# Kernel optimization log

Hardware: AMD Instinct MI355X
Metric: run time of the kernel (lower is better)

The kernel has to match this reference:

```python
import jax, jax.numpy as jnp
import numpy as np

N = 100000        # nodes
E = 1600000       # edges (before self-loops)
IN_CH = 256       # input features
HEADS = 8         # conv1 heads; per-head dim also 8 (GATConv(in, heads, heads=heads))
HID = 8
NCLASS = 64
SLOPE = 0.2       # PyG leaky_relu negative slope


def _gat_conv(x, edge_index, W, att_src, att_dst, bias, heads, ch, concat):
    """PyG GATConv (eval mode): gather -> leaky_relu score -> segment softmax -> scatter."""
    n = x.shape[0]
    src, dst = edge_index[0], edge_index[1]
    h = (x @ W).reshape(n, heads, ch)                      # [N, H, C]
    a_src = jnp.einsum('nhc,hc->nh', h, att_src)           # [N, H]
    a_dst = jnp.einsum('nhc,hc->nh', h, att_dst)
    alpha = jax.nn.leaky_relu(a_src[src] + a_dst[dst], SLOPE)  # [E, H]
    # segment softmax over destination node
    amax = jax.ops.segment_max(alpha, dst, num_segments=n)     # [N, H]
    ex = jnp.exp(alpha - amax[dst])
    denom = jax.ops.segment_sum(ex, dst, num_segments=n)
    coef = ex / (denom[dst] + 1e-16)                           # [E, H]
    out = jax.ops.segment_sum(coef[:, :, None] * h[src], dst, num_segments=n)  # [N, H, C]
    if concat:
        out = out.reshape(n, heads * ch)
    else:
        out = out.mean(axis=1)
    return out + bias


def _add_self_loops(edge_index, n):
    loop = jnp.arange(n, dtype=edge_index.dtype)
    return jnp.concatenate([edge_index, jnp.stack([loop, loop])], axis=1)


def setup_inputs() -> dict:
    key = jax.random.key(0)
    ks = jax.random.split(key, 10)
    g = lambda k, shp, s: (jax.random.normal(k, shp, jnp.float32) * s)
    return {
        'x': jax.random.normal(ks[0], (N, IN_CH), jnp.float32),
        'edge_index': jax.random.randint(ks[1], (2, E), 0, N, dtype=jnp.int64),
        'W1': g(ks[2], (IN_CH, HEADS * HID), 1.0 / np.sqrt(IN_CH)),
        'att_src1': g(ks[3], (HEADS, HID), 0.3),
        'att_dst1': g(ks[4], (HEADS, HID), 0.3),
        'b1': jnp.zeros((HEADS * HID,), jnp.float32),
        'W2': g(ks[5], (HEADS * HID, NCLASS), 1.0 / np.sqrt(HEADS * HID)),
        'att_src2': g(ks[6], (1, NCLASS), 0.3),
        'att_dst2': g(ks[7], (1, NCLASS), 0.3),
        'b2': jnp.zeros((NCLASS,), jnp.float32),
    }


def reference(x, edge_index, W1, att_src1, att_dst1, b1, W2, att_src2, att_dst2, b2):
    ei = _add_self_loops(edge_index, x.shape[0])
    h = jax.nn.elu(_gat_conv(x, ei, W1, att_src1, att_dst1, b1, HEADS, HID, True))
    # dropout is a no-op in eval mode
    h = _gat_conv(h, ei, W2, att_src2, att_dst2, b2, 1, NCLASS, False)
    return jax.nn.log_softmax(h, axis=-1)
```

## Files before the change

kernel.cpp:

```cpp
#include <hip/hip_runtime.h>
#include <hip/hip_bf16.h>

#define LRELU_SLOPE 0.2f
#define NBUK 256
#define BCAP 9728
#define CH2 6144

typedef unsigned int uint;
typedef unsigned short ushort;
typedef short bt8 __attribute__((ext_vector_type(8)));
typedef float fx4 __attribute__((ext_vector_type(4)));

__device__ __forceinline__ ushort f2bf(float f) {
    uint u = __float_as_uint(f);
    return (ushort)((u + 0x7FFF + ((u >> 16) & 1)) >> 16);
}
__device__ __forceinline__ float bf2f(ushort h) {
    return __uint_as_float(((uint)h) << 16);
}

#define ACC8(e, hv) \
    acc[0] += (e) * bf2f((ushort)((hv).x & 0xffff)); \
    acc[1] += (e) * bf2f((ushort)((hv).x >> 16));    \
    acc[2] += (e) * bf2f((ushort)((hv).y & 0xffff)); \
    acc[3] += (e) * bf2f((ushort)((hv).y >> 16));    \
    acc[4] += (e) * bf2f((ushort)((hv).z & 0xffff)); \
    acc[5] += (e) * bf2f((ushort)((hv).z >> 16));    \
    acc[6] += (e) * bf2f((ushort)((hv).w & 0xffff)); \
    acc[7] += (e) * bf2f((ushort)((hv).w >> 16));

#define EDGE_H8(sjv, LIVE) { \
    uint4 hv = *(const uint4*)(HB + (size_t)(sjv) * 64 + ol * 8); \
    float h0 = bf2f((ushort)(hv.x & 0xffff)), h1 = bf2f((ushort)(hv.x >> 16)); \
    float h2 = bf2f((ushort)(hv.y & 0xffff)), h3 = bf2f((ushort)(hv.y >> 16)); \
    float h4 = bf2f((ushort)(hv.z & 0xffff)), h5 = bf2f((ushort)(hv.z >> 16)); \
    float h6 = bf2f((ushort)(hv.w & 0xffff)), h7 = bf2f((ushort)(hv.w >> 16)); \
    float dt = h0*w0.x + h1*w0.y + h2*w0.z + h3*w0.w \
             + h4*w1.x + h5*w1.y + h6*w1.z + h7*w1.w; \
    float a_ = dt + adh; a_ = a_ > 0.f ? a_ : LRELU_SLOPE * a_; \
    float e = __expf(a_); \
    if (!(LIVE)) e = 0.f; \
    dsum += e; \
    acc[0] += e*h0; acc[1] += e*h1; acc[2] += e*h2; acc[3] += e*h3; \
    acc[4] += e*h4; acc[5] += e*h5; acc[6] += e*h6; acc[7] += e*h7; }

__global__ __launch_bounds__(256) void prep_init(
    const float* __restrict__ W1, const float* __restrict__ W2,
    ushort* __restrict__ WT1, ushort* __restrict__ WT2, int* __restrict__ pcur)
{
    int t = threadIdx.x;
    int idx = blockIdx.x * 256 + t;
    if (blockIdx.x == 0) pcur[t] = t * BCAP;
    if (idx < 64 * 256) {
        int c = idx >> 8, k = idx & 255;
        WT1[idx] = f2bf(W1[k * 64 + c]);
    }
    int i2 = idx - 64 * 256;
    if (i2 >= 0 && i2 < 64 * 64) {
        int c = i2 >> 6, k = i2 & 63;
        WT2[i2] = f2bf(W2[k * 64 + c]);
    }
}

__device__ __forceinline__ void partition_body(
    int bid, const int* __restrict__ ei, int E_, int ET,
    int* __restrict__ pcur, uint* __restrict__ pairs,
    int* lcnt, int* lsc, int* lplace, int* gpos)
{
    const int t = threadIdx.x;
    const int base = bid * CH2;
    const int total = min(CH2, ET - base);
    if (total <= 0) return;

    if (t < NBUK) lcnt[t] = 0;
    __syncthreads();

    uint pp[6]; int pk[6];
    #pragma unroll
    for (int i = 0; i < 6; ++i) {
        int idx = t + i * 1024;
        pk[i] = -1;
        if (idx < total) {
            int e = base + idx;
            int s, d;
            if (e < E_) { s = ei[e]; d = ei[E_ + e]; } else { s = d = e - E_; }
            pk[i] = d >> 9;
            pp[i] = (uint)s | ((uint)(d & 511) << 17);
            atomicAdd(&lcnt[pk[i]], 1);
        }
    }
    __syncthreads();

    if (t < NBUK) lsc[t] = lcnt[t];
    __syncthreads();
    for (int off = 1; off < NBUK; off <<= 1) {
        int add = 0;
        if (t < NBUK && t >= off) add = lsc[t - off];
        __syncthreads();
        if (t < NBUK) lsc[t] += add;
        __syncthreads();
    }
    if (t < NBUK) {
        int excl = lsc[t] - lcnt[t];
        lplace[t] = excl;
        int c = lcnt[t];
        gpos[t] = c ? (atomicAdd(&pcur[t], c) - excl) : 0;
    }
    __syncthreads();

    #pragma unroll
    for (int i = 0; i < 6; ++i) {
        if (pk[i] >= 0) {
            int slot = atomicAdd(&lplace[pk[i]], 1);
            pairs[gpos[pk[i]] + slot] = pp[i];
        }
    }
}

__device__ __forceinline__ void gemm1_body4(
    int gbid, const float* __restrict__ X, const ushort* __restrict__ WT,
    ushort* __restrict__ OUT, float* __restrict__ a_dst,
    const float* __restrict__ att_d, int nrows,
    ushort* wt_l, ushort* a_l)
{
    constexpr int K = 256, LDW = K + 8, NIT = K / 32;
    const int t = threadIdx.x;
    const int tt = t & 255;
    const int base = (gbid * 4 + (t >> 8)) * 64;

    for (int idx = t * 8; idx < 64 * K; idx += 1024 * 8) {
        int r = idx / K, c = idx % K;
        *(uint4*)&wt_l[r * LDW + c] = *(const uint4*)&WT[idx];
    }

    const int w = tt >> 6, l = tt & 63;
    const int frow = l & 15;
    const int kof = (l >> 4) * 8;
    fx4 acc[4] = {};
    float4 rv0, rv1;

    auto load_tile = [&](int k0) {
        int kq = (tt & 7) * 4;
        int r0 = (tt >> 3);
        int g0 = base + r0, g1 = base + r0 + 32;
        rv0 = make_float4(0.f, 0.f, 0.f, 0.f);
        rv1 = make_float4(0.f, 0.f, 0.f, 0.f);
        if (g0 < nrows) rv0 = *(const float4*)(X + (size_t)g0 * K + k0 + kq);
        if (g1 < nrows) rv1 = *(const float4*)(X + (size_t)g1 * K + k0 + kq);
    };
    auto store_tile = [&]() {
        int kq = (tt & 7) * 4;
        int r0 = (tt >> 3);
        ushort4 o0, o1;
        o0.x = f2bf(rv0.x); o0.y = f2bf(rv0.y); o0.z = f2bf(rv0.z); o0.w = f2bf(rv0.w);
        o1.x = f2bf(rv1.x); o1.y = f2bf(rv1.y); o1.z = f2bf(rv1.z); o1.w = f2bf(rv1.w);
        *(ushort4*)&a_l[r0 * 40 + kq] = o0;
        *(ushort4*)&a_l[(r0 + 32) * 40 + kq] = o1;
    };

    load_tile(0);
    store_tile();
    for (int it = 0; it < NIT; ++it) {
        if (it + 1 < NIT) load_tile((it + 1) * 32);
        __syncthreads();
        bt8 af = *(const bt8*)&a_l[(16 * w + frow) * 40 + kof];
        #pragma unroll
        for (int g = 0; g < 4; ++g) {
            bt8 bf = *(const bt8*)&wt_l[(16 * g + frow) * LDW + it * 32 + kof];
            acc[g] = __builtin_amdgcn_mfma_f32_16x16x32_bf16(af, bf, acc[g], 0, 0, 0);
        }
        __syncthreads();
        if (it + 1 < NIT) store_tile();
    }

    const int orow0 = base + 16 * w + (l >> 4) * 4;
    const int ocol = l & 15;
    #pragma unroll
    for (int g = 0; g < 4; ++g) {
        #pragma unroll
        for (int r4 = 0; r4 < 4; ++r4) {
            int gr = orow0 + r4;
            if (gr < nrows) OUT[(size_t)gr * 64 + 16 * g + ocol] = f2bf(acc[g][r4]);
        }
    }

    float ad_c[4];
    #pragma unroll
    for (int g = 0; g < 4; ++g) ad_c[g] = att_d[16 * g + ocol];
    #pragma unroll
    for (int r4 = 0; r4 < 4; ++r4) {
        int gr = orow0 + r4;
        #pragma unroll
        for (int g = 0; g < 4; ++g) {
            float pd = acc[g][r4] * ad_c[g];
            pd += __shfl_xor(pd, 1, 64);
            pd += __shfl_xor(pd, 2, 64);
            pd += __shfl_xor(pd, 4, 64);
            if ((l & 7) == 0 && gr < nrows) {
                int head = 2 * g + ((l >> 3) & 1);
                a_dst[(size_t)gr * 8 + head] = pd;
            }
        }
    }
}

__global__ __launch_bounds__(1024) void part_gemm1(
    const int* __restrict__ ei, int E_, int ET, int part_grid,
    int* __restrict__ pcur, uint* __restrict__ pairs,
    const float* __restrict__ x, const ushort* __restrict__ WT1,
    ushort* __restrict__ HB, float* __restrict__ a_d1,
    const float* __restrict__ att_d, int n)
{
    __shared__ int lcnt[NBUK], lsc[NBUK], lplace[NBUK], gpos[NBUK];
    __shared__ ushort wt_l[64 * 264];
    __shared__ ushort a_l4[4][64 * 40];
    if ((int)blockIdx.x < part_grid)
        partition_body(blockIdx.x, ei, E_, ET, pcur, pairs, lcnt, lsc, lplace, gpos);
    else
        gemm1_body4(blockIdx.x - part_grid, x, WT1, HB, a_d1,
                    att_d, n, wt_l, a_l4[threadIdx.x >> 8]);
}

__global__ __launch_bounds__(1024) void phase2_build(
    const uint* __restrict__ pairs, const int* __restrict__ pcur,
    int* __restrict__ rp, int* __restrict__ ssrc, int n, int nbuk_used)
{
    __shared__ int hist[512], cur[512], psc[NBUK];
    const int k = blockIdx.x;
    const int t = threadIdx.x;
    const int beg = k * BCAP;
    const int cnt = pcur[k] - beg;
    const int dbase = k << 9;

    if (t < 512) hist[t] = 0;
    if (t < NBUK) psc[t] = (t < nbuk_used) ? (pcur[t] - t * BCAP) : 0;
    __syncthreads();
    for (int off = 1; off < NBUK; off <<= 1) {
        int add = (t < NBUK && t >= off) ? psc[t - off] : 0;
        __syncthreads();
        if (t < NBUK) psc[t] += add;
        __syncthreads();
    }
    const int bbase = k ? psc[k - 1] : 0;

    for (int i = t; i < cnt; i += 1024)
        atomicAdd(&hist[pairs[beg + i] >> 17], 1);
    __syncthreads();

    int c0 = (t < 512) ? hist[t] : 0;
    for (int off = 1; off < 512; off <<= 1) {
        int add = (t < 512 && t >= off) ? hist[t - off] : 0;
        __syncthreads();
        if (t < 512) hist[t] += add;
        __syncthreads();
    }
    if (t < 512) {
        int node = dbase + t;
        if (node < n) rp[node] = bbase + hist[t];
        cur[t] = hist[t] - c0;
    }
    __syncthreads();

    for (int i = t; i < cnt; i += 1024) {
        uint p = pairs[beg + i];
        int j = p >> 17;
        int pos = bbase + atomicAdd(&cur[j], 1);
        ssrc[pos] = (int)(p & 0x1FFFF);
    }
}

__global__ __launch_bounds__(256) void gemm2_att(
    const ushort* __restrict__ X, const ushort* __restrict__ WT,
    ushort* __restrict__ OUT, float* __restrict__ a_src, float* __restrict__ a_dst,
    const float* __restrict__ att_s, const float* __restrict__ att_d, int nrows)
{
    constexpr int K = 64, LDW = K + 8, NIT = K / 32;
    __shared__ ushort wt_l[64 * LDW];
    __shared__ ushort a_l[64 * 40];
    const int t = threadIdx.x;
    const int base = blockIdx.x * 64;

    for (int idx = t * 8; idx < 64 * K; idx += 256 * 8) {
        int r = idx / K, c = idx % K;
        *(uint4*)&wt_l[r * LDW + c] = *(const uint4*)&WT[idx];
    }

    const int w = t >> 6, l = t & 63;
    const int frow = l & 15;
    const int kof = (l >> 4) * 8;
    fx4 acc[4] = {};
    uint4 rb;

    auto load_tile = [&](int k0) {
        int r = t >> 2, kq = (t & 3) * 8;
        int gr = base + r;
        rb = make_uint4(0, 0, 0, 0);
        if (gr < nrows) rb = *(const uint4*)(X + (size_t)gr * K + k0 + kq);
    };
    auto store_tile = [&]() {
        int r = t >> 2, kq = (t & 3) * 8;
        *(uint4*)&a_l[r * 40 + kq] = rb;
    };

    load_tile(0);
    store_tile();
    for (int it = 0; it < NIT; ++it) {
        if (it + 1 < NIT) load_tile((it + 1) * 32);
        __syncthreads();
        bt8 af = *(const bt8*)&a_l[(16 * w + frow) * 40 + kof];
        #pragma unroll
        for (int g = 0; g < 4; ++g) {
            bt8 bf = *(const bt8*)&wt_l[(16 * g + frow) * LDW + it * 32 + kof];
            acc[g] = __builtin_amdgcn_mfma_f32_16x16x32_bf16(af, bf, acc[g], 0, 0, 0);
        }
        __syncthreads();
        if (it + 1 < NIT) store_tile();
    }

    const int orow0 = base + 16 * w + (l >> 4) * 4;
    const int ocol = l & 15;
    #pragma unroll
    for (int g = 0; g < 4; ++g) {
        #pragma unroll
        for (int r4 = 0; r4 < 4; ++r4) {
            int gr = orow0 + r4;
            if (gr < nrows) OUT[(size_t)gr * 64 + 16 * g + ocol] = f2bf(acc[g][r4]);
        }
    }

    float as_c[4], ad_c[4];
    #pragma unroll
    for (int g = 0; g < 4; ++g) {
        as_c[g] = att_s[16 * g + ocol];
        ad_c[g] = att_d[16 * g + ocol];
    }
    #pragma unroll
    for (int r4 = 0; r4 < 4; ++r4) {
        int gr = orow0 + r4;
        float ps = 0.f, pd = 0.f;
        #pragma unroll
        for (int g = 0; g < 4; ++g) {
            ps += acc[g][r4] * as_c[g];
            pd += acc[g][r4] * ad_c[g];
        }
        ps += __shfl_xor(ps, 1, 64); pd += __shfl_xor(pd, 1, 64);
        ps += __shfl_xor(ps, 2, 64); pd += __shfl_xor(pd, 2, 64);
        ps += __shfl_xor(ps, 4, 64); pd += __shfl_xor(pd, 4, 64);
        ps += __shfl_xor(ps, 8, 64); pd += __shfl_xor(pd, 8, 64);
        if ((l & 15) == 0 && gr < nrows) {
            a_src[gr] = ps;
            a_dst[gr] = pd;
        }
    }
}

__global__ __launch_bounds__(256) void gather_h8(
    const int* __restrict__ rp, const int* __restrict__ ssrc,
    const float* __restrict__ a_dst, const float* __restrict__ att_s,
    const ushort* __restrict__ HB, const float* __restrict__ bias,
    ushort* __restrict__ HACT, int n)
{
    int node = blockIdx.x * 32 + (threadIdx.x >> 3);
    if (node >= n) return;
    int ol = threadIdx.x & 7;
    int end = rp[node];
    int start = node ? rp[node - 1] : 0;
    float adh = a_dst[(size_t)node * 8 + ol];
    float4 w0 = *(const float4*)(att_s + ol * 8);
    float4 w1 = *(const float4*)(att_s + ol * 8 + 4);
    float acc[8] = {};
    float dsum = 0.f;

    int i0 = start;
    for (; i0 + 8 <= end; i0 += 8) {
        int sv = ssrc[i0 + ol];
        #pragma unroll
        for (int j = 0; j < 8; ++j) {
            int sj = __shfl(sv, j, 8);
            EDGE_H8(sj, true);
        }
    }
    if (i0 < end) {
        int cnt = end - i0;
        int sv = (ol < cnt) ? ssrc[i0 + ol] : 0;
        #pragma unroll
        for (int j = 0; j < 8; ++j) {
            int sj = __shfl(sv, j, 8);
            EDGE_H8(sj, j < cnt);
        }
    }
    float inv = 1.f / (dsum + 1e-16f);
    float4 b0 = *(const float4*)(bias + ol * 8);
    float4 b1 = *(const float4*)(bias + ol * 8 + 4);
    float v[8];
    v[0] = acc[0] * inv + b0.x; v[1] = acc[1] * inv + b0.y;
    v[2] = acc[2] * inv + b0.z; v[3] = acc[3] * inv + b0.w;
    v[4] = acc[4] * inv + b1.x; v[5] = acc[5] * inv + b1.y;
    v[6] = acc[6] * inv + b1.z; v[7] = acc[7] * inv + b1.w;
    #pragma unroll
    for (int c = 0; c < 8; ++c) v[c] = v[c] > 0.f ? v[c] : expm1f(v[c]);
    uint4 o;
    o.x = (uint)f2bf(v[0]) | ((uint)f2bf(v[1]) << 16);
    o.y = (uint)f2bf(v[2]) | ((uint)f2bf(v[3]) << 16);
    o.z = (uint)f2bf(v[4]) | ((uint)f2bf(v[5]) << 16);
    o.w = (uint)f2bf(v[6]) | ((uint)f2bf(v[7]) << 16);
    *(uint4*)(HACT + (size_t)node * 64 + ol * 8) = o;
}

__global__ __launch_bounds__(256) void gather_h1_lsm(
    const int* __restrict__ rp, const int* __restrict__ ssrc,
    const float* __restrict__ a_src, const float* __restrict__ a_dst,
    const ushort* __restrict__ HB, const float* __restrict__ bias,
    float* __restrict__ OUT, int n)
{
    int node = blockIdx.x * 32 + (threadIdx.x >> 3);
    if (node >= n) return;
    int ol = threadIdx.x & 7;
    int end = rp[node];
    int start = node ? rp[node - 1] : 0;
    float ad = a_dst[node];
    float acc[8] = {};
    float dsum = 0.f;

    int i0 = start;
    for (; i0 + 16 <= end; i0 += 16) {
        int svA = ssrc[i0 + ol];
        int svB = ssrc[i0 + 8 + ol];
        #pragma unroll
        for (int j = 0; j < 8; ++j) {
            int sjA = __shfl(svA, j, 8);
            float aA = a_src[sjA] + ad;
            aA = aA > 0.f ? aA : LRELU_SLOPE * aA;
            float eA = __expf(aA);
            uint4 hvA = *(const uint4*)(HB + (size_t)sjA * 64 + ol * 8);
            dsum += eA; ACC8(eA, hvA);
            int sjB = __shfl(svB, j, 8);
            float aB = a_src[sjB] + ad;
            aB = aB > 0.f ? aB : LRELU_SLOPE * aB;
            float eB = __expf(aB);
            uint4 hvB = *(const uint4*)(HB + (size_t)sjB * 64 + ol * 8);
            dsum += eB; ACC8(eB, hvB);
        }
    }
    for (; i0 < end; i0 += 8) {
        int cnt = min(8, end - i0);
        int sv = (ol < cnt) ? ssrc[i0 + ol] : 0;
        #pragma unroll
        for (int j = 0; j < 8; ++j) {
            int sj = __shfl(sv, j, 8);
            float a = a_src[sj] + ad;
            a = a > 0.f ? a : LRELU_SLOPE * a;
            float e = __expf(a);
            e = (j < cnt) ? e : 0.f;
            uint4 hv = *(const uint4*)(HB + (size_t)sj * 64 + ol * 8);
            dsum += e; ACC8(e, hv);
        }
    }
    float inv = 1.f / (dsum + 1e-16f);
    float4 b0 = *(const float4*)(bias + ol * 8);
    float4 b1 = *(const float4*)(bias + ol * 8 + 4);
    float v[8];
    v[0] = acc[0] * inv + b0.x; v[1] = acc[1] * inv + b0.y;
    v[2] = acc[2] * inv + b0.z; v[3] = acc[3] * inv + b0.w;
    v[4] = acc[4] * inv + b1.x; v[5] = acc[5] * inv + b1.y;
    v[6] = acc[6] * inv + b1.z; v[7] = acc[7] * inv + b1.w;

    float m = v[0];
    #pragma unroll
    for (int c = 1; c < 8; ++c) m = fmaxf(m, v[c]);
    m = fmaxf(m, __shfl_xor(m, 1, 8));
    m = fmaxf(m, __shfl_xor(m, 2, 8));
    m = fmaxf(m, __shfl_xor(m, 4, 8));
    float s = 0.f;
    #pragma unroll
    for (int c = 0; c < 8; ++c) s += __expf(v[c] - m);
    s += __shfl_xor(s, 1, 8);
    s += __shfl_xor(s, 2, 8);
    s += __shfl_xor(s, 4, 8);
    float lse = m + __logf(s);
    float4 o0 = make_float4(v[0] - lse, v[1] - lse, v[2] - lse, v[3] - lse);
    float4 o1 = make_float4(v[4] - lse, v[5] - lse, v[6] - lse, v[7] - lse);
    *(float4*)(OUT + (size_t)node * 64 + ol * 8) = o0;
    *(float4*)(OUT + (size_t)node * 64 + ol * 8 + 4) = o1;
}

extern "C" void kernel_launch(void* const* d_in, const int* in_sizes, int n_in,
                              void* d_out, int out_size, void* d_ws, size_t ws_size,
                              hipStream_t stream)
{
    const float* x    = (const float*)d_in[0];
    const int*   ei   = (const int*)d_in[1];
    const float* W1   = (const float*)d_in[2];
    const float* as1w = (const float*)d_in[3];
    const float* ad1w = (const float*)d_in[4];
    const float* b1   = (const float*)d_in[5];
    const float* W2   = (const float*)d_in[6];
    const float* as2w = (const float*)d_in[7];
    const float* ad2w = (const float*)d_in[8];
    const float* b2   = (const float*)d_in[9];
    float* out = (float*)d_out;

    const int n  = in_sizes[0] / 256;
    const int E_ = in_sizes[1] / 2;
    const int ET = E_ + n;
    const int NBUKU = (n + 511) >> 9;

    char* wsb = (char*)d_ws;
    uint*   pairs= (uint*)wsb;
    ushort* HB   = (ushort*)(pairs + (size_t)NBUK*BCAP);
    ushort* HACT = HB + (size_t)n * 64;
    float*  a_d1 = (float*)(HACT + (size_t)n * 64);
    float*  a_s2 = a_d1 + (size_t)n * 8;
    float*  a_d2 = a_s2 + n;
    int*    rp   = (int*)(a_d2 + n);
    int*    pcur = rp + n;
    int*    ssrc = pcur + NBUK;
    ushort* WT1  = (ushort*)(ssrc + ET);
    ushort* WT2  = WT1 + 64 * 256;

    const int gemm_grid  = (n + 63) / 64;
    const int gemm_grid4 = (n + 255) / 256;
    const int gath_grid  = (n + 31) / 32;
    const int part_grid  = (ET + CH2 - 1) / CH2;

    prep_init<<<80, 256, 0, stream>>>(W1, W2, WT1, WT2, pcur);
    part_gemm1<<<part_grid + gemm_grid4, 1024, 0, stream>>>(
        ei, E_, ET, part_grid, pcur, pairs, x, WT1, HB, a_d1, ad1w, n);
    phase2_build<<<NBUKU, 1024, 0, stream>>>(pairs, pcur, rp, ssrc, n, NBUKU);
    gather_h8<<<gath_grid, 256, 0, stream>>>(rp, ssrc, a_d1, as1w, HB, b1, HACT, n);
    gemm2_att<<<gemm_grid, 256, 0, stream>>>(HACT, WT2, HB, a_s2, a_d2, as2w, ad2w, n);
    gather_h1_lsm<<<gath_grid, 256, 0, stream>>>(rp, ssrc, a_s2, a_d2, HB, b2, out, n);
}
```

Measured before the change: 166.9 us.

## Split fused partition+GEMM1 kernel and load X rows directly into MFMA registers

Undoes the heterogeneous fused launch that ran edge partitioning and the first GEMM in one grid, giving each its own kernel, with GEMM1 now launched after phase2_build. GEMM1 becomes a 256-thread block that preloads each lane's whole X row slice into registers and converts to bf16 in-register, dropping the shared-memory A tile staging and per-iteration barriers. This trades the concurrency of the fused launch for simpler kernels, lower LDS use and higher occupancy. It adds an extra launch, and the 16 float4 registers per thread raise register pressure.

```diff
diff --git a/kernel.cpp b/kernel.cpp
--- a/kernel.cpp
+++ b/kernel.cpp
@@ -62,13 +62,13 @@
     }
 }
 
-__device__ __forceinline__ void partition_body(
-    int bid, const int* __restrict__ ei, int E_, int ET,
-    int* __restrict__ pcur, uint* __restrict__ pairs,
-    int* lcnt, int* lsc, int* lplace, int* gpos)
-{
+__global__ __launch_bounds__(1024) void partition_pairs(
+    const int* __restrict__ ei, int E_, int ET,
+    int* __restrict__ pcur, uint* __restrict__ pairs)
+{
+    __shared__ int lcnt[NBUK], lsc[NBUK], lplace[NBUK], gpos[NBUK];
     const int t = threadIdx.x;
-    const int base = bid * CH2;
+    const int base = blockIdx.x * CH2;
     const int total = min(CH2, ET - base);
     if (total <= 0) return;
 
@@ -117,60 +117,51 @@
     }
 }
 
-__device__ __forceinline__ void gemm1_body4(
-    int gbid, const float* __restrict__ X, const ushort* __restrict__ WT,
+__global__ __launch_bounds__(256) void gemm1_att(
+    const float* __restrict__ X, const ushort* __restrict__ WT,
     ushort* __restrict__ OUT, float* __restrict__ a_dst,
-    const float* __restrict__ att_d, int nrows,
-    ushort* wt_l, ushort* a_l)
+    const float* __restrict__ att_d, int nrows)
 {
     constexpr int K = 256, LDW = K + 8, NIT = K / 32;
+    __shared__ ushort wt_l[64 * LDW];
     const int t = threadIdx.x;
-    const int tt = t & 255;
-    const int base = (gbid * 4 + (t >> 8)) * 64;
-
-    for (int idx = t * 8; idx < 64 * K; idx += 1024 * 8) {
+    const int base = blockIdx.x * 64;
+
+    for (int idx = t * 8; idx < 64 * K; idx += 256 * 8) {
         int r = idx / K, c = idx % K;
         *(uint4*)&wt_l[r * LDW + c] = *(const uint4*)&WT[idx];
     }
-
-    const int w = tt >> 6, l = tt & 63;
+    __syncthreads();
+
+    const int w = t >> 6, l = t & 63;
     const int frow = l & 15;
     const int kof = (l >> 4) * 8;
+    const int arow = base + 16 * w + frow;
+    const bool rowok = arow < nrows;
+    const float4* xrow = (const float4*)(X + (size_t)arow * K + kof);
     fx4 acc[4] = {};
-    float4 rv0, rv1;
-
-    auto load_tile = [&](int k0) {
-        int kq = (tt & 7) * 4;
-        int r0 = (tt >> 3);
-        int g0 = base + r0, g1 = base + r0 + 32;
-        rv0 = make_float4(0.f, 0.f, 0.f, 0.f);
-        rv1 = make_float4(0.f, 0.f, 0.f, 0.f);
-        if (g0 < nrows) rv0 = *(const float4*)(X + (size_t)g0 * K + k0 + kq);
-        if (g1 < nrows) rv1 = *(const float4*)(X + (size_t)g1 * K + k0 + kq);
-    };
-    auto store_tile = [&]() {
-        int kq = (tt & 7) * 4;
-        int r0 = (tt >> 3);
-        ushort4 o0, o1;
-        o0.x = f2bf(rv0.x); o0.y = f2bf(rv0.y); o0.z = f2bf(rv0.z); o0.w = f2bf(rv0.w);
-        o1.x = f2bf(rv1.x); o1.y = f2bf(rv1.y); o1.z = f2bf(rv1.z); o1.w = f2bf(rv1.w);
-        *(ushort4*)&a_l[r0 * 40 + kq] = o0;
-        *(ushort4*)&a_l[(r0 + 32) * 40 + kq] = o1;
-    };
-
-    load_tile(0);
-    store_tile();
+
+    float4 rx[16];
+    const float4 z4 = make_float4(0.f, 0.f, 0.f, 0.f);
+    #pragma unroll
     for (int it = 0; it < NIT; ++it) {
-        if (it + 1 < NIT) load_tile((it + 1) * 32);
-        __syncthreads();
-        bt8 af = *(const bt8*)&a_l[(16 * w + frow) * 40 + kof];
+        rx[2 * it]     = rowok ? xrow[it * 8]     : z4;
+        rx[2 * it + 1] = rowok ? xrow[it * 8 + 1] : z4;
+    }
+
+    #pragma unroll
+    for (int it = 0; it < NIT; ++it) {
+        float4 c0 = rx[2 * it], c1 = rx[2 * it + 1];
+        bt8 af;
+        af[0] = (short)f2bf(c0.x); af[1] = (short)f2bf(c0.y);
+        af[2] = (short)f2bf(c0.z); af[3] = (short)f2bf(c0.w);
+        af[4] = (short)f2bf(c1.x); af[5] = (short)f2bf(c1.y);
+        af[6] = (short)f2bf(c1.z); af[7] = (short)f2bf(c1.w);
         #pragma unroll
         for (int g = 0; g < 4; ++g) {
             bt8 bf = *(const bt8*)&wt_l[(16 * g + frow) * LDW + it * 32 + kof];
             acc[g] = __builtin_amdgcn_mfma_f32_16x16x32_bf16(af, bf, acc[g], 0, 0, 0);
         }
-        __syncthreads();
-        if (it + 1 < NIT) store_tile();
     }
 
     const int orow0 = base + 16 * w + (l >> 4) * 4;
@@ -202,23 +193,6 @@
             }
         }
     }
-}
-
-__global__ __launch_bounds__(1024) void part_gemm1(
-    const int* __restrict__ ei, int E_, int ET, int part_grid,
-    int* __restrict__ pcur, uint* __restrict__ pairs,
-    const float* __restrict__ x, const ushort* __restrict__ WT1,
-    ushort* __restrict__ HB, float* __restrict__ a_d1,
-    const float* __restrict__ att_d, int n)
-{
-    __shared__ int lcnt[NBUK], lsc[NBUK], lplace[NBUK], gpos[NBUK];
-    __shared__ ushort wt_l[64 * 264];
-    __shared__ ushort a_l4[4][64 * 40];
-    if ((int)blockIdx.x < part_grid)
-        partition_body(blockIdx.x, ei, E_, ET, pcur, pairs, lcnt, lsc, lplace, gpos);
-    else
-        gemm1_body4(blockIdx.x - part_grid, x, WT1, HB, a_d1,
-                    att_d, n, wt_l, a_l4[threadIdx.x >> 8]);
 }
 
 __global__ __launch_bounds__(1024) void phase2_build(
@@ -518,15 +492,14 @@
     ushort* WT1  = (ushort*)(ssrc + ET);
     ushort* WT2  = WT1 + 64 * 256;
 
-    const int gemm_grid  = (n + 63) / 64;
-    const int gemm_grid4 = (n + 255) / 256;
-    const int gath_grid  = (n + 31) / 32;
-    const int part_grid  = (ET + CH2 - 1) / CH2;
+    const int gemm_grid = (n + 63) / 64;
+    const int gath_grid = (n + 31) / 32;
+    const int part_grid = (ET + CH2 - 1) / CH2;
 
     prep_init<<<80, 256, 0, stream>>>(W1, W2, WT1, WT2, pcur);
-    part_gemm1<<<part_grid + gemm_grid4, 1024, 0, stream>>>(
-        ei, E_, ET, part_grid, pcur, pairs, x, WT1, HB, a_d1, ad1w, n);
+    partition_pairs<<<part_grid, 1024, 0, stream>>>(ei, E_, ET, pcur, pairs);
     phase2_build<<<NBUKU, 1024, 0, stream>>>(pairs, pcur, rp, ssrc, n, NBUKU);
+    gemm1_att<<<gemm_grid, 256, 0, stream>>>(x, WT1, HB, a_d1, ad1w, n);
     gather_h8<<<gath_grid, 256, 0, stream>>>(rp, ssrc, a_d1, as1w, HB, b1, HACT, n);
     gemm2_att<<<gemm_grid, 256, 0, stream>>>(HACT, WT2, HB, a_s2, a_d2, as2w, ad2w, n);
     gather_h1_lsm<<<gath_grid, 256, 0, stream>>>(rp, ssrc, a_s2, a_d2, HB, b2, out, n);
```

New measurement: 187.4 us. +12.3%, slower.
